# Performance work log

Measured on AMD Instinct MI355X. Metric: run time of the kernel, lower is better.

Reference implementation:

```python
import jax, jax.numpy as jnp
import numpy as np

ORDER = 3  # AnovaKernel(order=3)


def setup_inputs() -> dict:
    key = jax.random.key(0)
    x = jax.random.normal(key, (8192, 64, 64), dtype=jnp.float32)
    return {"x": x}


def reference(x):
    """ANOVA kernel via elementary-symmetric-polynomial DP.

    x: (B, F, E). Returns (B,).
    a_prev has field-axis length F+1 (row 0 is the t=0 boundary of ones).
    """
    bsz, nfield, nemb = x.shape
    a_prev = jnp.ones((bsz, nfield + 1, nemb), dtype=x.dtype)
    a = a_prev
    for t in range(ORDER):
        # term[:, j] = x[:, t+j] * a_prev[:, t+j]  for j in [0, F-t)
        term = x[:, t:, :] * a_prev[:, t:-1, :]
        # pad t+1 zero rows at the front of the field axis, then prefix-sum
        padded = jnp.pad(term, ((0, 0), (t + 1, 0), (0, 0)))
        a = jnp.cumsum(padded, axis=1)
        a_prev = a
    return jnp.sum(a[:, -1, :], axis=-1)
```

## Files before the change

kernel.cpp:

```cpp
#include <hip/hip_runtime.h>


constexpr int BATCH = 8192;
constexpr int NFIELD = 64;
constexpr int NEMB = 64;

__global__ __launch_bounds__(256) void anova3_kernel(const float* __restrict__ x,
                                                     float* __restrict__ out) {
    const int tid = blockIdx.x * 256 + threadIdx.x;
    const int b = tid >> 4;
    const int g = tid & 15;

    const float4* xp = reinterpret_cast<const float4*>(x)
                     + (size_t)b * (NFIELD * NEMB / 4) + g;

    float4 s1 = make_float4(0.f, 0.f, 0.f, 0.f);
    float4 s2 = make_float4(0.f, 0.f, 0.f, 0.f);
    float4 s3 = make_float4(0.f, 0.f, 0.f, 0.f);

#pragma unroll 16
    for (int f = 0; f < NFIELD; ++f) {
        float4 v = xp[(size_t)f * (NEMB / 4)];
        s3.x = fmaf(s2.x, v.x, s3.x); s2.x = fmaf(s1.x, v.x, s2.x); s1.x += v.x;
        s3.y = fmaf(s2.y, v.y, s3.y); s2.y = fmaf(s1.y, v.y, s2.y); s1.y += v.y;
        s3.z = fmaf(s2.z, v.z, s3.z); s2.z = fmaf(s1.z, v.z, s2.z); s1.z += v.z;
        s3.w = fmaf(s2.w, v.w, s3.w); s2.w = fmaf(s1.w, v.w, s2.w); s1.w += v.w;
    }

    float r = (s3.x + s3.y) + (s3.z + s3.w);
    r += __shfl_xor(r, 8);
    r += __shfl_xor(r, 4);
    r += __shfl_xor(r, 2);
    r += __shfl_xor(r, 1);

    if (g == 0) out[b] = r;
}

extern "C" void kernel_launch(void* const* d_in, const int* in_sizes, int n_in,
                              void* d_out, int out_size, void* d_ws, size_t ws_size,
                              hipStream_t stream) {
    const float* x = (const float*)d_in[0];
    float* out = (float*)d_out;
    const int total_threads = BATCH * 16;
    dim3 grid(total_threads / 256);
    anova3_kernel<<<grid, dim3(256), 0, stream>>>(x, out);
}
```

Measured before the change: 185.8 us.

## Split field axis across four lane groups and merge symmetric polynomials via shuffles

Each batch row is now handled by a full 64-lane wavefront, with four groups of 16 lanes each processing 16 fields. The partial elementary symmetric sums are combined with a cross-lane polynomial-product merge using xor shuffles. This quadruples thread count and shortens serial dependency chains to expose more memory-level parallelism. It adds shuffle and merge arithmetic, and the floating-point summation order changes.

```diff
diff --git a/kernel.cpp b/kernel.cpp
--- a/kernel.cpp
+++ b/kernel.cpp
@@ -2,38 +2,62 @@
 
 
 constexpr int BATCH = 8192;
-constexpr int NFIELD = 64;
-constexpr int NEMB = 64;
+
+__device__ inline float4 shfl_xor4(float4 v, int d) {
+    float4 r;
+    r.x = __shfl_xor(v.x, d);
+    r.y = __shfl_xor(v.y, d);
+    r.z = __shfl_xor(v.z, d);
+    r.w = __shfl_xor(v.w, d);
+    return r;
+}
 
 __global__ __launch_bounds__(256) void anova3_kernel(const float* __restrict__ x,
                                                      float* __restrict__ out) {
-    const int tid = blockIdx.x * 256 + threadIdx.x;
-    const int b = tid >> 4;
-    const int g = tid & 15;
+    const int tid  = blockIdx.x * 256 + threadIdx.x;
+    const int lane = threadIdx.x & 63;
+    const int b    = tid >> 6;
+    const int g    = lane & 15;
+    const int h    = lane >> 4;
 
     const float4* xp = reinterpret_cast<const float4*>(x)
-                     + (size_t)b * (NFIELD * NEMB / 4) + g;
+                     + (size_t)b * 1024 + (size_t)h * 256 + g;
 
     float4 s1 = make_float4(0.f, 0.f, 0.f, 0.f);
-    float4 s2 = make_float4(0.f, 0.f, 0.f, 0.f);
-    float4 s3 = make_float4(0.f, 0.f, 0.f, 0.f);
+    float4 s2 = s1, s3 = s1;
 
-#pragma unroll 16
-    for (int f = 0; f < NFIELD; ++f) {
-        float4 v = xp[(size_t)f * (NEMB / 4)];
+#pragma unroll
+    for (int f = 0; f < 16; ++f) {
+        float4 v = xp[f * 16];
         s3.x = fmaf(s2.x, v.x, s3.x); s2.x = fmaf(s1.x, v.x, s2.x); s1.x += v.x;
         s3.y = fmaf(s2.y, v.y, s3.y); s2.y = fmaf(s1.y, v.y, s2.y); s1.y += v.y;
         s3.z = fmaf(s2.z, v.z, s3.z); s2.z = fmaf(s1.z, v.z, s2.z); s1.z += v.z;
         s3.w = fmaf(s2.w, v.w, s3.w); s2.w = fmaf(s1.w, v.w, s2.w); s1.w += v.w;
     }
 
+#pragma unroll
+    for (int d = 16; d <= 32; d <<= 1) {
+        float4 o1 = shfl_xor4(s1, d);
+        float4 o2 = shfl_xor4(s2, d);
+        float4 o3 = shfl_xor4(s3, d);
+        s3.x += o3.x + s2.x * o1.x + s1.x * o2.x;
+        s3.y += o3.y + s2.y * o1.y + s1.y * o2.y;
+        s3.z += o3.z + s2.z * o1.z + s1.z * o2.z;
+        s3.w += o3.w + s2.w * o1.w + s1.w * o2.w;
+        s2.x += o2.x + s1.x * o1.x;
+        s2.y += o2.y + s1.y * o1.y;
+        s2.z += o2.z + s1.z * o1.z;
+        s2.w += o2.w + s1.w * o1.w;
+        s1.x += o1.x; s1.y += o1.y; s1.z += o1.z; s1.w += o1.w;
+    }
+
     float r = (s3.x + s3.y) + (s3.z + s3.w);
+    r += __shfl_xor(r, 1);
+    r += __shfl_xor(r, 2);
+    r += __shfl_xor(r, 4);
     r += __shfl_xor(r, 8);
-    r += __shfl_xor(r, 4);
-    r += __shfl_xor(r, 2);
-    r += __shfl_xor(r, 1);
 
-    if (g == 0) out[b] = r;
+    if (lane == 0) out[b] = r;
 }
 
 extern "C" void kernel_launch(void* const* d_in, const int* in_sizes, int n_in,
@@ -41,7 +65,7 @@
                               hipStream_t stream) {
     const float* x = (const float*)d_in[0];
     float* out = (float*)d_out;
-    const int total_threads = BATCH * 16;
+    const int total_threads = BATCH * 64;
     dim3 grid(total_threads / 256);
     anova3_kernel<<<grid, dim3(256), 0, stream>>>(x, out);
 }
```

Measured after the change: 187.5 us. About the same (+0.9%).
